# Performance work log

Measured on AMD Instinct MI355X. Metric: run time of the kernel, lower is better.

## Reference

```python
import jax, jax.numpy as jnp
import numpy as np

B, N, F_IN, F_OUT = 8, 2048, 256, 256
NEG_SLOPE = 0.2
EPS = 1e-7


def setup_inputs() -> dict:
    key = jax.random.key(0)
    k1, k2, k3, k4, k5 = jax.random.split(key, 5)
    x = jax.random.normal(k1, (B, N, F_IN), dtype=jnp.float32)
    # A is a 0/1 adjacency mask used as float in the module
    A = jax.random.bernoulli(k2, 0.5, (B, N, N)).astype(jnp.float32)
    # W: xavier_normal_ init, shape [in_features, out_features]
    W = jax.random.normal(k3, (F_IN, F_OUT), dtype=jnp.float32) * np.sqrt(2.0 / (F_IN + F_OUT))
    # attention_mechanism: Linear(2*F_OUT, 1) -> weight vector [2*F_OUT], scalar bias
    bound = 1.0 / np.sqrt(2 * F_OUT)
    a_w = jax.random.uniform(k4, (2 * F_OUT,), dtype=jnp.float32, minval=-bound, maxval=bound)
    a_b = jax.random.uniform(k5, (), dtype=jnp.float32, minval=-bound, maxval=bound)
    return {"A": A, "x": x, "W": W, "a_w": a_w, "a_b": a_b}


def reference(A, x, W, a_w, a_b):
    # Wh = x @ W : [B, N, F_OUT]
    Wh = jnp.einsum('bnf,fo->bno', x, W)
    # Linear([Wh_i ; Wh_j]) == Wh_i @ a_w[:F] + Wh_j @ a_w[F:] + b  (no O(N^2 F) concat)
    s_src = Wh @ a_w[:F_OUT]   # [B, N] contribution of row index i
    s_dst = Wh @ a_w[F_OUT:]   # [B, N] contribution of col index j
    e = s_src[:, :, None] + s_dst[:, None, :] + a_b  # [B, N, N]
    e = jnp.where(e > 0, e, NEG_SLOPE * e)           # leaky_relu(0.2)
    # masked softmax over dim=1 (as in the original module)
    exps = jnp.exp(e) * A
    sums = jnp.sum(exps, axis=1, keepdims=True) + EPS
    attn = exps / sums                                # [B, N, N]
    return jnp.einsum('bij,bjo->bio', attn, Wh)       # [B, N, F_OUT]
```

## Files before the change

### kernel.cpp

```cpp
#include <hip/hip_runtime.h>
#include <hip/hip_bf16.h>

#define NN 2048
#define BB 8
#define FD 256
#define NEG_SLOPE 0.2f
#define EPSV 1e-7f
#define PSTR 36

typedef __bf16 bf16x8 __attribute__((ext_vector_type(8)));
typedef __bf16 bf16x4 __attribute__((ext_vector_type(4)));
typedef __bf16 bf16x2 __attribute__((ext_vector_type(2)));
typedef float f32x4 __attribute__((ext_vector_type(4)));

__device__ __forceinline__ void gload16(const __bf16* g, __bf16* l) {
    __builtin_amdgcn_global_load_lds((const __attribute__((address_space(1))) unsigned int*)g,
                                     (__attribute__((address_space(3))) unsigned int*)l,
                                     16, 0, 0);
}

__global__ __launch_bounds__(256) void k1_prep(const float* __restrict__ W,
                                               __bf16* __restrict__ WT) {
    int idx = blockIdx.x * 256 + threadIdx.x;
    int o = idx >> 8, f = idx & 255;
    WT[idx] = (__bf16)W[f * FD + o];
}

__global__ __launch_bounds__(256) void k2_whgemm(const float* __restrict__ x,
                                                 const __bf16* __restrict__ WT,
                                                 const float* __restrict__ a_w,
                                                 float* __restrict__ Wh,
                                                 float* __restrict__ s_src,
                                                 float* __restrict__ s_dst) {
    const int wave = threadIdx.x >> 6;
    const int lane = threadIdx.x & 63;
    const int row0 = blockIdx.x * 32 + (wave >> 1) * 16;
    const int ohalf = (wave & 1) * 128;
    const int m = lane & 15;
    const int quad = lane >> 4;
    const int row = row0 + m;
    const float* xrow = x + (size_t)row * FD + quad * 8;

    f32x4 acc[8];
#pragma unroll
    for (int n = 0; n < 8; ++n) acc[n] = (f32x4){0.f, 0.f, 0.f, 0.f};

    for (int k0 = 0; k0 < FD; k0 += 32) {
        float4 xa = *(const float4*)(xrow + k0);
        float4 xb = *(const float4*)(xrow + k0 + 4);
        bf16x8 af;
        af[0] = (__bf16)xa.x; af[1] = (__bf16)xa.y; af[2] = (__bf16)xa.z; af[3] = (__bf16)xa.w;
        af[4] = (__bf16)xb.x; af[5] = (__bf16)xb.y; af[6] = (__bf16)xb.z; af[7] = (__bf16)xb.w;
#pragma unroll
        for (int n = 0; n < 8; ++n) {
            int o = ohalf + n * 16 + m;
            bf16x8 bf = *(const bf16x8*)(WT + o * FD + k0 + quad * 8);
            acc[n] = __builtin_amdgcn_mfma_f32_16x16x32_bf16(af, bf, acc[n], 0, 0, 0);
        }
    }
#pragma unroll
    for (int n = 0; n < 8; ++n) {
        int o = ohalf + n * 16 + m;
#pragma unroll
        for (int r = 0; r < 4; ++r) {
            Wh[(size_t)(row0 + quad * 4 + r) * FD + o] = acc[n][r];
        }
    }

    float psrc[4] = {0.f, 0.f, 0.f, 0.f};
    float pdst[4] = {0.f, 0.f, 0.f, 0.f};
#pragma unroll
    for (int n = 0; n < 8; ++n) {
        int o = ohalf + n * 16 + m;
        float awS = a_w[o], awD = a_w[FD + o];
#pragma unroll
        for (int r = 0; r < 4; ++r) {
            psrc[r] += acc[n][r] * awS;
            pdst[r] += acc[n][r] * awD;
        }
    }
#pragma unroll
    for (int off = 1; off <= 8; off <<= 1) {
#pragma unroll
        for (int r = 0; r < 4; ++r) {
            psrc[r] += __shfl_xor(psrc[r], off, 64);
            pdst[r] += __shfl_xor(pdst[r], off, 64);
        }
    }
    __shared__ float sS[2][2][16], sD[2][2][16];
    if (m == 0) {
        int rp = wave >> 1, oh = wave & 1;
#pragma unroll
        for (int r = 0; r < 4; ++r) {
            sS[rp][oh][quad * 4 + r] = psrc[r];
            sD[rp][oh][quad * 4 + r] = pdst[r];
        }
    }
    __syncthreads();
    if (threadIdx.x < 32) {
        int rp = threadIdx.x >> 4, idx = threadIdx.x & 15;
        int orow = blockIdx.x * 32 + rp * 16 + idx;
        s_src[orow] = sS[rp][0][idx] + sS[rp][1][idx];
        s_dst[orow] = sD[rp][0][idx] + sD[rp][1][idx];
    }
}

__global__ __launch_bounds__(256) void k4_den(const float* __restrict__ A,
                                              const float* __restrict__ s_src,
                                              const float* __restrict__ s_dst,
                                              const float* __restrict__ a_bp,
                                              float* __restrict__ den_part) {
    const int blk = blockIdx.x;
    const int b = blk & 7;
    const int jhalf = (blk >> 3) & 1;
    const int isp = blk >> 4;
    const int i0 = isp * 32;
    const int j = jhalf * 1024 + threadIdx.x * 4;
    __shared__ float ss[32];
    if (threadIdx.x < 32) ss[threadIdx.x] = s_src[b * NN + i0 + threadIdx.x] + a_bp[0];
    __syncthreads();
    float4 sd = *(const float4*)(s_dst + b * NN + j);
    float ax = 0.f, ay = 0.f, az = 0.f, aw = 0.f;
    const float* Ap = A + ((size_t)b * NN + i0) * NN + j;
#pragma unroll 8
    for (int i = 0; i < 32; ++i) {
        float4 a = *(const float4*)(Ap + (size_t)i * NN);
        float si = ss[i];
        float e0 = si + sd.x; e0 = e0 > 0.f ? e0 : NEG_SLOPE * e0;
        float e1 = si + sd.y; e1 = e1 > 0.f ? e1 : NEG_SLOPE * e1;
        float e2 = si + sd.z; e2 = e2 > 0.f ? e2 : NEG_SLOPE * e2;
        float e3 = si + sd.w; e3 = e3 > 0.f ? e3 : NEG_SLOPE * e3;
        ax += a.x * __expf(e0);
        ay += a.y * __expf(e1);
        az += a.z * __expf(e2);
        aw += a.w * __expf(e3);
    }
    float4 r = (float4){ax, ay, az, aw};
    *(float4*)(den_part + (size_t)isp * (BB * NN) + b * NN + j) = r;
}

__global__ __launch_bounds__(256) void k5_wht(const float* __restrict__ Wh,
                                              const float* __restrict__ den_part,
                                              __bf16* __restrict__ WhT) {
    const int b = blockIdx.z;
    const int j0 = blockIdx.x * 64;
    const int o0 = blockIdx.y * 64;
    __shared__ float tile[64][65];
    __shared__ float invd[64];
    if (threadIdx.x < 64) {
        float s = 0.f;
        const float* dp = den_part + b * NN + j0 + threadIdx.x;
#pragma unroll 8
        for (int sI = 0; sI < 64; ++sI) s += dp[(size_t)sI * (BB * NN)];
        invd[threadIdx.x] = 1.f / (s + EPSV);
    }
    __syncthreads();
    int jr = threadIdx.x >> 4, oc = (threadIdx.x & 15) * 4;
#pragma unroll
    for (int p = 0; p < 4; ++p) {
        int jj = jr + p * 16;
        float4 v = *(const float4*)(Wh + (size_t)(b * NN + j0 + jj) * FD + o0 + oc);
        float s = invd[jj];
        tile[jj][oc + 0] = v.x * s;
        tile[jj][oc + 1] = v.y * s;
        tile[jj][oc + 2] = v.z * s;
        tile[jj][oc + 3] = v.w * s;
    }
    __syncthreads();
    int ow = threadIdx.x >> 4, jc = (threadIdx.x & 15) * 4;
#pragma unroll
    for (int p = 0; p < 4; ++p) {
        int o = ow + p * 16;
        bf16x4 wv;
        wv[0] = (__bf16)tile[jc + 0][o];
        wv[1] = (__bf16)tile[jc + 1][o];
        wv[2] = (__bf16)tile[jc + 2][o];
        wv[3] = (__bf16)tile[jc + 3][o];
        *(bf16x4*)(WhT + (size_t)(b * FD + o0 + o) * NN + j0 + jc) = wv;
    }
}

__global__ __launch_bounds__(512) void k6_out(const float* __restrict__ A,
                                              const __bf16* __restrict__ WhT,
                                              const float* __restrict__ s_src,
                                              const float* __restrict__ s_dst,
                                              const float* __restrict__ a_bp,
                                              float* __restrict__ out) {
    __shared__ __bf16 Pt[2][32 * PSTR];
    __shared__ __bf16 Bt[2][256 * 32];
    const int blk = blockIdx.x;
    const int b = blk & 7;
    const int itile = blk >> 3;
    const int i0 = itile * 32;
    const int t = threadIdx.x;
    const int w = t >> 6, lane = t & 63;
    const int m = lane & 15, quad = lane >> 4;
    const int wrow = w >> 2, wcol = w & 3;

    const int prow = t >> 4, pjc = (t & 15) * 2;
    const float ssr = s_src[b * NN + i0 + prow] + a_bp[0];
    const float* Abase = A + ((size_t)(b * NN + i0 + prow)) * NN + pjc;
    const float* sdbase = s_dst + b * NN + pjc;
    __bf16* Pw = &Pt[0][0] + prow * PSTR + pjc;
    const int pstep = 32 * PSTR;

    const int srow = t >> 2, schunk = t & 3;
    const __bf16* gB = WhT + ((size_t)(b * FD + srow)) * NN + schunk * 8;
    __bf16* lB = &Bt[0][0] + (w * 16) * 32;
    const int lstepB = 256 * 32;

    float2 a0 = *(const float2*)(Abase);
    float2 q0 = *(const float2*)(sdbase);
    gload16(gB, lB);
    gload16(gB + (size_t)128 * NN, lB + 128 * 32);

#define BUILD_P(dstbuf)                                                          \
    {                                                                            \
        bf16x2 pv; float e;                                                      \
        e = ssr + q0.x; e = e > 0.f ? e : NEG_SLOPE * e; pv[0] = (__bf16)(a0.x * __expf(e)); \
        e = ssr + q0.y; e = e > 0.f ? e : NEG_SLOPE * e; pv[1] = (__bf16)(a0.y * __expf(e)); \
        *(bf16x2*)(Pw + (dstbuf) * pstep) = pv;                                  \
    }

    BUILD_P(0)

    f32x4 acc[4];
#pragma unroll
    for (int n = 0; n < 4; ++n) acc[n] = (f32x4){0.f, 0.f, 0.f, 0.f};

    const __bf16* Pr = &Pt[0][0] + (wrow * 16 + m) * PSTR + quad * 8;
    const __bf16* Br = &Bt[0][0] + (wcol * 64 + m) * 32 + quad * 8;

    for (int kk = 0; kk < 64; ++kk) {
        __syncthreads();
        const int cur = kk & 1, nb = cur ^ 1;
        if (kk < 63) {
            gload16(gB + (kk + 1) * 32, lB + nb * lstepB);
            gload16(gB + (size_t)128 * NN + (kk + 1) * 32, lB + nb * lstepB + 128 * 32);
            a0 = *(const float2*)(Abase + (kk + 1) * 32);
            q0 = *(const float2*)(sdbase + (kk + 1) * 32);
        }
        const __bf16* Pk = Pr + cur * pstep;
        const __bf16* Bk = Br + cur * lstepB;
        bf16x8 af = *(const bf16x8*)(Pk);
#pragma unroll
        for (int n = 0; n < 4; ++n) {
            bf16x8 bfr = *(const bf16x8*)(Bk + n * 16 * 32);
            acc[n] = __builtin_amdgcn_mfma_f32_16x16x32_bf16(af, bfr, acc[n], 0, 0, 0);
        }
        if (kk < 63) BUILD_P(nb)
    }

#pragma unroll
    for (int n = 0; n < 4; ++n) {
        int o = wcol * 64 + n * 16 + m;
#pragma unroll
        for (int rr = 0; rr < 4; ++rr) {
            int orow = i0 + wrow * 16 + quad * 4 + rr;
            out[((size_t)b * NN + orow) * FD + o] = acc[n][rr];
        }
    }
#undef BUILD_P
}

extern "C" void kernel_launch(void* const* d_in, const int* in_sizes, int n_in,
                              void* d_out, int out_size, void* d_ws, size_t ws_size,
                              hipStream_t stream) {
    const float* A   = (const float*)d_in[0];
    const float* x   = (const float*)d_in[1];
    const float* W   = (const float*)d_in[2];
    const float* a_w = (const float*)d_in[3];
    const float* a_b = (const float*)d_in[4];
    float* out = (float*)d_out;

    char* ws = (char*)d_ws;
    __bf16* WT      = (__bf16*)ws;
    float*  Wh      = (float*)(ws + 131072);
    __bf16* WhT     = (__bf16*)(ws + 16908288);
    float*  s_src   = (float*)(ws + 25296896);
    float*  s_dst   = (float*)(ws + 25362432);
    float*  den_part= (float*)(ws + 25427968);

    k1_prep<<<256, 256, 0, stream>>>(W, WT);
    k2_whgemm<<<512, 256, 0, stream>>>(x, WT, a_w, Wh, s_src, s_dst);
    k4_den<<<1024, 256, 0, stream>>>(A, s_src, s_dst, a_b, den_part);
    k5_wht<<<dim3(32, 4, 8), 256, 0, stream>>>(Wh, den_part, WhT);
    k6_out<<<512, 512, 0, stream>>>(A, WhT, s_src, s_dst, a_b, out);
}
```

Measured before the change: 303.6 us.

## Split k6 output columns into halves with 256-thread blocks and wider P loads

The attention-output kernel now tiles the 256 output features into two 128-column halves. It launches 1024 blocks of 256 threads instead of 512 blocks of 512, which halves the LDS for the WhT tile per block. Each thread now builds four P entries from float4 loads of A and s_dst instead of two. The cost is that every block still reads and exponentiates its full 32-row slab of A, so A traffic and exp work are duplicated across the two feature halves, in exchange for more blocks and lower per-block resource use.

```diff
diff --git a/kernel.cpp b/kernel.cpp
--- a/kernel.cpp
+++ b/kernel.cpp
@@ -10,7 +10,6 @@
 
 typedef __bf16 bf16x8 __attribute__((ext_vector_type(8)));
 typedef __bf16 bf16x4 __attribute__((ext_vector_type(4)));
-typedef __bf16 bf16x2 __attribute__((ext_vector_type(2)));
 typedef float f32x4 __attribute__((ext_vector_type(4)));
 
 __device__ __forceinline__ void gload16(const __bf16* g, __bf16* l) {
@@ -180,46 +179,52 @@
     }
 }
 
-__global__ __launch_bounds__(512) void k6_out(const float* __restrict__ A,
+__global__ __launch_bounds__(256) void k6_out(const float* __restrict__ A,
                                               const __bf16* __restrict__ WhT,
                                               const float* __restrict__ s_src,
                                               const float* __restrict__ s_dst,
                                               const float* __restrict__ a_bp,
                                               float* __restrict__ out) {
     __shared__ __bf16 Pt[2][32 * PSTR];
-    __shared__ __bf16 Bt[2][256 * 32];
+    __shared__ __bf16 Bt[2][128 * 32];
     const int blk = blockIdx.x;
     const int b = blk & 7;
-    const int itile = blk >> 3;
+    const int r_ = blk >> 3;
+    const int itile = r_ & 63;
+    const int oh = r_ >> 6;
     const int i0 = itile * 32;
+    const int o0 = oh * 128;
     const int t = threadIdx.x;
     const int w = t >> 6, lane = t & 63;
     const int m = lane & 15, quad = lane >> 4;
-    const int wrow = w >> 2, wcol = w & 3;
-
-    const int prow = t >> 4, pjc = (t & 15) * 2;
+    const int wrow = w >> 1, wcol = w & 1;
+
+    const int prow = t >> 3, pj = (t & 7) * 4;
     const float ssr = s_src[b * NN + i0 + prow] + a_bp[0];
-    const float* Abase = A + ((size_t)(b * NN + i0 + prow)) * NN + pjc;
-    const float* sdbase = s_dst + b * NN + pjc;
-    __bf16* Pw = &Pt[0][0] + prow * PSTR + pjc;
+    const float* Abase = A + ((size_t)(b * NN + i0 + prow)) * NN + pj;
+    const float* sdbase = s_dst + b * NN + pj;
+    __bf16* Pw = &Pt[0][0] + prow * PSTR + pj;
     const int pstep = 32 * PSTR;
 
-    const int srow = t >> 2, schunk = t & 3;
-    const __bf16* gB = WhT + ((size_t)(b * FD + srow)) * NN + schunk * 8;
-    __bf16* lB = &Bt[0][0] + (w * 16) * 32;
-    const int lstepB = 256 * 32;
-
-    float2 a0 = *(const float2*)(Abase);
-    float2 q0 = *(const float2*)(sdbase);
-    gload16(gB, lB);
-    gload16(gB + (size_t)128 * NN, lB + 128 * 32);
+    const __bf16* gB0 = WhT + ((size_t)(b * FD + o0 + w * 16 + (lane >> 2))) * NN + (lane & 3) * 8;
+    const __bf16* gB1 = gB0 + (size_t)64 * NN;
+    __bf16* lB0 = &Bt[0][0] + (w * 16) * 32;
+    __bf16* lB1 = &Bt[0][0] + (w * 16 + 64) * 32;
+    const int lstepB = 128 * 32;
+
+    float4 a0 = *(const float4*)(Abase);
+    float4 q0 = *(const float4*)(sdbase);
+    gload16(gB0, lB0);
+    gload16(gB1, lB1);
 
 #define BUILD_P(dstbuf)                                                          \
     {                                                                            \
-        bf16x2 pv; float e;                                                      \
+        bf16x4 pv; float e;                                                      \
         e = ssr + q0.x; e = e > 0.f ? e : NEG_SLOPE * e; pv[0] = (__bf16)(a0.x * __expf(e)); \
         e = ssr + q0.y; e = e > 0.f ? e : NEG_SLOPE * e; pv[1] = (__bf16)(a0.y * __expf(e)); \
-        *(bf16x2*)(Pw + (dstbuf) * pstep) = pv;                                  \
+        e = ssr + q0.z; e = e > 0.f ? e : NEG_SLOPE * e; pv[2] = (__bf16)(a0.z * __expf(e)); \
+        e = ssr + q0.w; e = e > 0.f ? e : NEG_SLOPE * e; pv[3] = (__bf16)(a0.w * __expf(e)); \
+        *(bf16x4*)(Pw + (dstbuf) * pstep) = pv;                                  \
     }
 
     BUILD_P(0)
@@ -235,10 +240,10 @@
         __syncthreads();
         const int cur = kk & 1, nb = cur ^ 1;
         if (kk < 63) {
-            gload16(gB + (kk + 1) * 32, lB + nb * lstepB);
-            gload16(gB + (size_t)128 * NN + (kk + 1) * 32, lB + nb * lstepB + 128 * 32);
-            a0 = *(const float2*)(Abase + (kk + 1) * 32);
-            q0 = *(const float2*)(sdbase + (kk + 1) * 32);
+            gload16(gB0 + (kk + 1) * 32, lB0 + nb * lstepB);
+            gload16(gB1 + (kk + 1) * 32, lB1 + nb * lstepB);
+            a0 = *(const float4*)(Abase + (kk + 1) * 32);
+            q0 = *(const float4*)(sdbase + (kk + 1) * 32);
         }
         const __bf16* Pk = Pr + cur * pstep;
         const __bf16* Bk = Br + cur * lstepB;
@@ -253,7 +258,7 @@
 
 #pragma unroll
     for (int n = 0; n < 4; ++n) {
-        int o = wcol * 64 + n * 16 + m;
+        int o = o0 + wcol * 64 + n * 16 + m;
 #pragma unroll
         for (int rr = 0; rr < 4; ++rr) {
             int orow = i0 + wrow * 16 + quad * 4 + rr;
@@ -285,5 +290,5 @@
     k2_whgemm<<<512, 256, 0, stream>>>(x, WT, a_w, Wh, s_src, s_dst);
     k4_den<<<1024, 256, 0, stream>>>(A, s_src, s_dst, a_b, den_part);
     k5_wht<<<dim3(32, 4, 8), 256, 0, stream>>>(Wh, den_part, WhT);
-    k6_out<<<512, 512, 0, stream>>>(A, WhT, s_src, s_dst, a_b, out);
-}
+    k6_out<<<1024, 256, 0, stream>>>(A, WhT, s_src, s_dst, a_b, out);
+}
```

Measured after the change: 298.0 us. About the same (-1.9%).
